# Optimization experiments

Hardware: AMD Instinct MI355X
Metric: run time of the kernel (lower is better)

The kernel has to match this reference:

```python
import jax, jax.numpy as jnp
import numpy as np

N_EMBD = 1024
N_HEAD = 16
LORA_R = 8
LORA_ALPHA = 16
SCALE = LORA_ALPHA / LORA_R


def lora_linear(x, W, b, A, Bm):
    # loralib: F.linear(x, W, b) + (x @ A.T @ B.T) * scaling
    return x @ W.T + b + ((x @ A.T) @ Bm.T) * SCALE


def setup_inputs() -> dict:
    key = jax.random.key(0)
    ks = jax.random.split(key, 9)
    B, T, C = 4, 2048, N_EMBD
    s_in = 1.0 / np.sqrt(C)
    x = jax.random.normal(ks[0], (B, T, C), dtype=jnp.float32)
    Wqkv = jax.random.normal(ks[1], (3 * C, C), dtype=jnp.float32) * s_in
    bqkv = jnp.zeros((3 * C,), dtype=jnp.float32)
    Aqkv = jax.random.normal(ks[2], (LORA_R, C), dtype=jnp.float32) * s_in
    Bqkv = jnp.zeros((3 * C, LORA_R), dtype=jnp.float32)  # loralib inits B to zero
    Wproj = jax.random.normal(ks[3], (C, C), dtype=jnp.float32) * s_in
    bproj = jnp.zeros((C,), dtype=jnp.float32)
    Aproj = jax.random.normal(ks[4], (LORA_R, C), dtype=jnp.float32) * s_in
    Bproj = jnp.zeros((C, LORA_R), dtype=jnp.float32)
    return {"x": x, "Wqkv": Wqkv, "bqkv": bqkv, "Aqkv": Aqkv, "Bqkv": Bqkv,
            "Wproj": Wproj, "bproj": bproj, "Aproj": Aproj, "Bproj": Bproj}


def reference(x, Wqkv, bqkv, Aqkv, Bqkv, Wproj, bproj, Aproj, Bproj):
    B, T, C = x.shape
    H, D = N_HEAD, C // N_HEAD
    qkv = lora_linear(x, Wqkv, bqkv, Aqkv, Bqkv)  # [B,T,3C]
    q, k, v = jnp.split(qkv, 3, axis=2)
    # [B,T,C] -> [B,H,T,D]
    q = q.reshape(B, T, H, D).transpose(0, 2, 1, 3)
    k = k.reshape(B, T, H, D).transpose(0, 2, 1, 3)
    v = v.reshape(B, T, H, D).transpose(0, 2, 1, 3)
    att = jnp.einsum("bhqd,bhkd->bhqk", q, k) * (1.0 / np.sqrt(D))
    causal = jnp.tril(jnp.ones((T, T), dtype=bool))
    att = jnp.where(causal[None, None], att, jnp.float32(-jnp.inf))
    att = jax.nn.softmax(att, axis=-1)
    out = jnp.einsum("bhqk,bhkd->bhqd", att, v)  # [B,H,T,D]
    out = out.transpose(0, 2, 1, 3).reshape(B, T, C)
    return lora_linear(out, Wproj, bproj, Aproj, Bproj)
```

## Files before the change

kernel.cpp:

```cpp
#include <hip/hip_runtime.h>
#include <hip/hip_bf16.h>

typedef __bf16 bf16_t;
typedef __bf16 bf16x8 __attribute__((ext_vector_type(8)));
typedef __bf16 bf16x4 __attribute__((ext_vector_type(4)));
typedef float  f32x4  __attribute__((ext_vector_type(4)));

#define MFMA_BF16 __builtin_amdgcn_mfma_f32_16x16x32_bf16
#define NEG_BIG  (-3.0e38f)

#if __has_builtin(__builtin_amdgcn_exp2f)
#define EXP2F(x) __builtin_amdgcn_exp2f(x)
#else
#define EXP2F(x) exp2f(x)
#endif

#define SBAR()       __builtin_amdgcn_s_barrier()
#define SCHED0()     __builtin_amdgcn_sched_barrier(0)
#define WAIT_LGKM0() asm volatile("s_waitcnt lgkmcnt(0)" ::: "memory")
#define WAIT_LGKM8() asm volatile("s_waitcnt lgkmcnt(8)" ::: "memory")
#define WAIT_VM0()   asm volatile("s_waitcnt vmcnt(0)" ::: "memory")
#define WAIT_VM4()   asm volatile("s_waitcnt vmcnt(4)" ::: "memory")
#define WAIT_VM6()   asm volatile("s_waitcnt vmcnt(6)" ::: "memory")

__device__ __forceinline__ void load16_lds(const bf16_t* g, bf16_t* l) {
    __builtin_amdgcn_global_load_lds(
        (const __attribute__((address_space(1))) void*)g,
        (__attribute__((address_space(3))) void*)l, 16, 0, 0);
}

__device__ inline bf16x8 ld8(const bf16_t* p) { return *(const bf16x8*)p; }
__device__ inline bf16x8 ld8(const float* p) {
    f32x4 a = *(const f32x4*)p;
    f32x4 b = *(const f32x4*)(p + 4);
    bf16x8 o;
    o[0] = (bf16_t)a[0]; o[1] = (bf16_t)a[1]; o[2] = (bf16_t)a[2]; o[3] = (bf16_t)a[3];
    o[4] = (bf16_t)b[0]; o[5] = (bf16_t)b[1]; o[6] = (bf16_t)b[2]; o[7] = (bf16_t)b[3];
    return o;
}

template <typename TX>
__device__ __forceinline__ void lora_xa_body(
    const TX* __restrict__ X, const float* __restrict__ A,
    float* __restrict__ out, int m, int lane)
{
    const TX* xp = X + (size_t)m * 1024;
    float acc[8];
#pragma unroll
    for (int r = 0; r < 8; r++) acc[r] = 0.f;

#pragma unroll 4
    for (int ci = 0; ci < 16; ci++) {
        int k = ci * 64 + lane;
        float xv = (float)xp[k];
#pragma unroll
        for (int r = 0; r < 8; r++) acc[r] += xv * A[r * 1024 + k];
    }
#pragma unroll
    for (int r = 0; r < 8; r++) {
        float v = acc[r];
        v += __shfl_xor(v, 1);  v += __shfl_xor(v, 2);  v += __shfl_xor(v, 4);
        v += __shfl_xor(v, 8);  v += __shfl_xor(v, 16); v += __shfl_xor(v, 32);
        if (lane == 0) out[m * 8 + r] = v;
    }
}

template <typename TX>
__global__ __launch_bounds__(256) void lora_xa_kernel(
    const TX* __restrict__ X, const float* __restrict__ A,
    float* __restrict__ out)
{
    const int lane = threadIdx.x & 63;
    const int w    = threadIdx.x >> 6;
    const int m    = blockIdx.x * 4 + w;
    lora_xa_body<TX>(X, A, out, m, lane);
}

__global__ __launch_bounds__(256) void prep_kernel(
    const float* __restrict__ x, const float* __restrict__ Wqkv,
    const float* __restrict__ Wproj,
    bf16_t* __restrict__ x16, bf16_t* __restrict__ Wqkv16,
    bf16_t* __restrict__ Wproj16,
    const float* __restrict__ Aqkv, float* __restrict__ xa1)
{
    const int bid = blockIdx.x;
    if (bid < 6144) {
        const float* in; bf16_t* out; size_t off;
        if (bid < 4096)      { in = x;     out = x16;     off = (size_t)bid * 2048; }
        else if (bid < 5632) { in = Wqkv;  out = Wqkv16;  off = (size_t)(bid - 4096) * 2048; }
        else                 { in = Wproj; out = Wproj16; off = (size_t)(bid - 5632) * 2048; }
        size_t i = off + (size_t)threadIdx.x * 8;
        *(bf16x8*)&out[i] = ld8(&in[i]);
    } else {
        const int lane = threadIdx.x & 63;
        const int w    = threadIdx.x >> 6;
        const int m    = (bid - 6144) * 4 + w;
        lora_xa_body<float>(x, Aqkv, xa1, m, lane);
    }
}

__device__ __forceinline__ void gemm_epilogue(
    f32x4 (&acc)[4][4], const float* bias, const float* xA, const float* LB,
    bf16_t* C0, bf16_t* C1, bf16_t* C2, float* Cf,
    int tile_m, int tile_n, int wm, int wn, int c, int g)
{
    const int seg    = tile_n >> 10;
    const int tn_loc = tile_n & 1023;
    bf16_t* Cout = (seg == 0) ? C0 : (seg == 1) ? C1 : C2;

    float biasf[4];
    float lbv[4][8];
#pragma unroll
    for (int j = 0; j < 4; j++) {
        int col = tile_n + wn + j * 16 + c;
        biasf[j] = bias[col];
        f32x4 lb0 = *(const f32x4*)&LB[(size_t)col * 8];
        f32x4 lb1 = *(const f32x4*)&LB[(size_t)col * 8 + 4];
#pragma unroll
        for (int r = 0; r < 4; r++) { lbv[j][r] = lb0[r]; lbv[j][r + 4] = lb1[r]; }
    }
#pragma unroll
    for (int i = 0; i < 4; i++) {
#pragma unroll
        for (int rg = 0; rg < 4; rg++) {
            int row = tile_m + wm + i * 16 + g * 4 + rg;
            f32x4 xa0 = *(const f32x4*)&xA[(size_t)row * 8];
            f32x4 xa1 = *(const f32x4*)&xA[(size_t)row * 8 + 4];
#pragma unroll
            for (int j = 0; j < 4; j++) {
                float lora = xa0[0] * lbv[j][0] + xa0[1] * lbv[j][1] +
                             xa0[2] * lbv[j][2] + xa0[3] * lbv[j][3] +
                             xa1[0] * lbv[j][4] + xa1[1] * lbv[j][5] +
                             xa1[2] * lbv[j][6] + xa1[3] * lbv[j][7];
                float v = acc[i][j][rg] + biasf[j] + 2.0f * lora;
                int lcol = tn_loc + wn + j * 16 + c;
                if (Cf) Cf[(size_t)row * 1024 + lcol] = v;
                else    Cout[(size_t)row * 1024 + lcol] = (bf16_t)v;
            }
        }
    }
}

template <typename TA, typename TW>
__global__ __launch_bounds__(256) void gemm_bias_lora(
    const TA* __restrict__ A, const TW* __restrict__ W,
    const float* __restrict__ bias, const float* __restrict__ xA,
    const float* __restrict__ LB,
    bf16_t* __restrict__ C0, bf16_t* __restrict__ C1, bf16_t* __restrict__ C2,
    float* __restrict__ Cf, int K)
{
    __shared__ __align__(16) bf16_t As[128 * 72];
    __shared__ __align__(16) bf16_t Bs[128 * 72];

    const int t    = threadIdx.x;
    const int lane = t & 63;
    const int w    = t >> 6;
    const int wm   = (w >> 1) * 64;
    const int wn   = (w & 1) * 64;
    const int c    = lane & 15;
    const int g    = lane >> 4;
    const int tile_m = blockIdx.y * 128;
    const int tile_n = blockIdx.x * 128;

    const int srow = t >> 3;
    const int scol = (t & 7) * 8;

    f32x4 acc[4][4];
#pragma unroll
    for (int i = 0; i < 4; i++)
#pragma unroll
        for (int j = 0; j < 4; j++) {
            f32x4 z = {0.f, 0.f, 0.f, 0.f};
            acc[i][j] = z;
        }

    for (int k0 = 0; k0 < K; k0 += 64) {
#pragma unroll
        for (int i = 0; i < 4; i++) {
            int r = srow + i * 32;
            *(bf16x8*)&As[r * 72 + scol] = ld8(&A[(size_t)(tile_m + r) * K + k0 + scol]);
            *(bf16x8*)&Bs[r * 72 + scol] = ld8(&W[(size_t)(tile_n + r) * K + k0 + scol]);
        }
        __syncthreads();

#pragma unroll
        for (int kk = 0; kk < 2; kk++) {
            bf16x8 af[4], bfr[4];
#pragma unroll
            for (int i = 0; i < 4; i++)
                af[i] = *(const bf16x8*)&As[(wm + i * 16 + c) * 72 + kk * 32 + g * 8];
#pragma unroll
            for (int j = 0; j < 4; j++)
                bfr[j] = *(const bf16x8*)&Bs[(wn + j * 16 + c) * 72 + kk * 32 + g * 8];
#pragma unroll
            for (int i = 0; i < 4; i++)
#pragma unroll
                for (int j = 0; j < 4; j++)
                    acc[i][j] = MFMA_BF16(af[i], bfr[j], acc[i][j], 0, 0, 0);
        }
        __syncthreads();
    }
    gemm_epilogue(acc, bias, xA, LB, C0, C1, C2, Cf, tile_m, tile_n, wm, wn, c, g);
}

#define AS_OFF(row, q) ((row) * 64 + (((q) ^ ((row) & 7)) * 8))

__global__ __launch_bounds__(256) void gemm_proj_fused(
    const bf16_t* __restrict__ A, const bf16_t* __restrict__ W,
    const float* __restrict__ bias, const float* __restrict__ Ap,
    const float* __restrict__ LB, float* __restrict__ Cf, int K)
{
    __shared__ __align__(16) bf16_t As[128 * 64];
    __shared__ __align__(16) bf16_t Bs[128 * 64];
    __shared__ __align__(16) bf16_t Ap16[8 * 1032];

    const int t    = threadIdx.x;
    const int lane = t & 63;
    const int w    = t >> 6;
    const int wm   = (w >> 1) * 64;
    const int wn   = (w & 1) * 64;
    const int c    = lane & 15;
    const int g    = lane >> 4;
    const int tile_m = blockIdx.y * 128;
    const int tile_n = blockIdx.x * 128;

    {
        int r = t >> 5;
        int k = (t & 31) * 32;
        const float* src = Ap + (size_t)r * 1024 + k;
        bf16_t* dst = &Ap16[r * 1032 + k];
#pragma unroll
        for (int e = 0; e < 32; e += 8)
            *(bf16x8*)&dst[e] = ld8(&src[e]);
    }

    const int trow = t >> 3;
    const int k8   = (t & 7) ^ (trow & 7);
    const bf16_t* Ab = A + (size_t)tile_m * K + k8 * 8;
    const bf16_t* Wb = W + (size_t)tile_n * K + k8 * 8;

    f32x4 acc[4][4];
#pragma unroll
    for (int i = 0; i < 4; i++)
#pragma unroll
        for (int j = 0; j < 4; j++) {
            f32x4 z = {0.f, 0.f, 0.f, 0.f};
            acc[i][j] = z;
        }
    f32x4 accx[2];
    {
        f32x4 z = {0.f, 0.f, 0.f, 0.f};
        accx[0] = z; accx[1] = z;
    }

    for (int k0 = 0; k0 < K; k0 += 64) {
#pragma unroll
        for (int i = 0; i < 4; i++) {
            int row = i * 32 + trow;
            load16_lds(&Ab[(size_t)row * K + k0], &As[(i * 256 + t) * 8]);
            load16_lds(&Wb[(size_t)row * K + k0], &Bs[(i * 256 + t) * 8]);
        }
        __syncthreads();

#pragma unroll
        for (int kk = 0; kk < 2; kk++) {
            bf16x8 af[4], bfr[4];
#pragma unroll
            for (int i = 0; i < 4; i++)
                af[i] = *(const bf16x8*)&As[AS_OFF(wm + i * 16 + c, kk * 4 + g)];
#pragma unroll
            for (int j = 0; j < 4; j++)
                bfr[j] = *(const bf16x8*)&Bs[AS_OFF(wn + j * 16 + c, kk * 4 + g)];
#pragma unroll
            for (int i = 0; i < 4; i++)
#pragma unroll
                for (int j = 0; j < 4; j++)
                    acc[i][j] = MFMA_BF16(af[i], bfr[j], acc[i][j], 0, 0, 0);
            bf16x8 apf = *(const bf16x8*)&Ap16[(c & 7) * 1032 + k0 + kk * 32 + g * 8];
#pragma unroll
            for (int fi = 0; fi < 2; fi++) {
                bf16x8 xf = *(const bf16x8*)&As[AS_OFF(w * 32 + fi * 16 + c, kk * 4 + g)];
                accx[fi] = MFMA_BF16(xf, apf, accx[fi], 0, 0, 0);
            }
        }
        __syncthreads();
    }

    float* xa2l = (float*)As;
    if (c < 8) {
#pragma unroll
        for (int fi = 0; fi < 2; fi++)
#pragma unroll
            for (int rg = 0; rg < 4; rg++)
                xa2l[(w * 32 + fi * 16 + g * 4 + rg) * 8 + c] = accx[fi][rg];
    }
    __syncthreads();

    float biasf[4];
    float lbv[4][8];
#pragma unroll
    for (int j = 0; j < 4; j++) {
        int col = tile_n + wn + j * 16 + c;
        biasf[j] = bias[col];
        f32x4 lb0 = *(const f32x4*)&LB[(size_t)col * 8];
        f32x4 lb1 = *(const f32x4*)&LB[(size_t)col * 8 + 4];
#pragma unroll
        for (int r = 0; r < 4; r++) { lbv[j][r] = lb0[r]; lbv[j][r + 4] = lb1[r]; }
    }
#pragma unroll
    for (int i = 0; i < 4; i++) {
#pragma unroll
        for (int rg = 0; rg < 4; rg++) {
            int rloc = wm + i * 16 + g * 4 + rg;
            int row  = tile_m + rloc;
            f32x4 xa0 = *(const f32x4*)&xa2l[rloc * 8];
            f32x4 xa1 = *(const f32x4*)&xa2l[rloc * 8 + 4];
#pragma unroll
            for (int j = 0; j < 4; j++) {
                float lora = xa0[0] * lbv[j][0] + xa0[1] * lbv[j][1] +
                             xa0[2] * lbv[j][2] + xa0[3] * lbv[j][3] +
                             xa1[0] * lbv[j][4] + xa1[1] * lbv[j][5] +
                             xa1[2] * lbv[j][6] + xa1[3] * lbv[j][7];
                float v = acc[i][j][rg] + biasf[j] + 2.0f * lora;
                Cf[(size_t)row * 1024 + tile_n + wn + j * 16 + c] = v;
            }
        }
    }
}

__global__ __launch_bounds__(512, 2) void gemm_256(
    const bf16_t* __restrict__ A, const bf16_t* __restrict__ W,
    const float* __restrict__ bias, const float* __restrict__ Aq,
    const float* __restrict__ LB,
    bf16_t* __restrict__ C0, bf16_t* __restrict__ C1, bf16_t* __restrict__ C2,
    float* __restrict__ Cf, int K, int ntn)
{
    __shared__ __align__(16) bf16_t As[4][8192];
    __shared__ __align__(16) bf16_t Bs[4][8192];
    __shared__ __align__(16) bf16_t Aq16[8 * 1032];

    const int t    = threadIdx.x;
    const int lane = t & 63;
    const int w    = t >> 6;
    const int c    = lane & 15;
    const int g    = lane >> 4;

    const int nwg = gridDim.x;
    const int cpx = nwg >> 3;
    const int bid = blockIdx.x;
    const int swz = (bid & 7) * cpx + (bid >> 3);
    const int tile_m = (swz / ntn) * 256;
    const int tile_n = (swz % ntn) * 256;

    const int wm  = (w >> 2) * 128;
    const int wn  = (w & 3) * 64;
    const int ha  = w >> 2;
    const int hb  = wn >> 7;
    const int wnl = wn & 127;

    {
        int r = t >> 6;
        int k = (t & 63) * 16;
        const float* src = Aq + (size_t)r * 1024 + k;
        bf16_t* dst = &Aq16[r * 1032 + k];
        *(bf16x8*)&dst[0] = ld8(&src[0]);
        *(bf16x8*)&dst[8] = ld8(&src[8]);
    }

    int aoffs[8][2], boffs[4][2];
#pragma unroll
    for (int il = 0; il < 8; il++) {
        int rl = il * 16 + c;
#pragma unroll
        for (int ks = 0; ks < 2; ks++)
            aoffs[il][ks] = rl * 64 + (((ks * 4 + g) ^ (rl & 7)) * 8);
    }
#pragma unroll
    for (int j2 = 0; j2 < 4; j2++) {
        int rl = wnl + j2 * 16 + c;
#pragma unroll
        for (int ks = 0; ks < 2; ks++)
            boffs[j2][ks] = rl * 64 + (((ks * 4 + g) ^ (rl & 7)) * 8);
    }

    const int xrow0 = (w & 3) * 32;
    int xoffs[2][2];
#pragma unroll
    for (int fi = 0; fi < 2; fi++) {
        int rl = xrow0 + fi * 16 + c;
#pragma unroll
        for (int ks = 0; ks < 2; ks++)
            xoffs[fi][ks] = rl * 64 + (((ks * 4 + g) ^ (rl & 7)) * 8);
    }

    const int trow = t >> 3;
    const int qq   = (t & 7) ^ (trow & 7);
    const bf16_t* aO = A + (size_t)(tile_m + trow) * K + qq * 8;
    const bf16_t* wO = W + (size_t)(tile_n + trow) * K + qq * 8;
    const size_t rK64 = (size_t)64 * K;

#define STAGE_A(T, h) do {                                                         \
    load16_lds(aO + (size_t)(h) * 128 * K + (size_t)(T) * 64,                      \
               &As[((T) & 1) * 2 + (h)][t * 8]);                                   \
    load16_lds(aO + (size_t)(h) * 128 * K + rK64 + (size_t)(T) * 64,               \
               &As[((T) & 1) * 2 + (h)][4096 + t * 8]); } while (0)
#define STAGE_B(T, h) do {                                                         \
    load16_lds(wO + (size_t)(h) * 128 * K + (size_t)(T) * 64,                      \
               &Bs[((T) & 1) * 2 + (h)][t * 8]);                                   \
    load16_lds(wO + (size_t)(h) * 128 * K + rK64 + (size_t)(T) * 64,               \
               &Bs[((T) & 1) * 2 + (h)][4096 + t * 8]); } while (0)

    f32x4 acc[8][4];
#pragma unroll
    for (int i = 0; i < 8; i++)
#pragma unroll
        for (int j2 = 0; j2 < 4; j2++) {
            f32x4 z = {0.f, 0.f, 0.f, 0.f};
            acc[i][j2] = z;
        }
    f32x4 accx[2];
    {
        f32x4 z = {0.f, 0.f, 0.f, 0.f};
        accx[0] = z; accx[1] = z;
    }

    const int NT = K >> 6;

    STAGE_B(0, 0); STAGE_B(0, 1); STAGE_A(0, 0); STAGE_A(0, 1);
    WAIT_VM4();
    STAGE_B(1, 0); STAGE_B(1, 1); STAGE_A(1, 0);
    WAIT_LGKM0();
    WAIT_VM6();
    SBAR();

    for (int j = 0; j < NT; j++) {
        const bf16_t* Ab = &As[(j & 1) * 2 + ha][0];
        const bf16_t* Bb = &Bs[(j & 1) * 2 + hb][0];
        bf16x8 bfr[4][2], af0[4], af1[4];
        bf16x8 xf0a, xf1a, xf0b, xf1b, apf0, apf1;

#pragma unroll
        for (int j2 = 0; j2 < 4; j2++) {
            bfr[j2][0] = *(const bf16x8*)&Bb[boffs[j2][0]];
            bfr[j2][1] = *(const bf16x8*)&Bb[boffs[j2][1]];
        }
#pragma unroll
        for (int i = 0; i < 4; i++) af0[i] = *(const bf16x8*)&Ab[aoffs[i][0]];
        if (j + 1 < NT) STAGE_A(j + 1, 1);
        WAIT_LGKM8();
        SBAR();
        WAIT_LGKM0();
        SCHED0();
        __builtin_amdgcn_s_setprio(1);
#pragma unroll
        for (int i = 0; i < 4; i++)
#pragma unroll
            for (int j2 = 0; j2 < 4; j2++)
                acc[i][j2] = MFMA_BF16(af0[i], bfr[j2][0], acc[i][j2], 0, 0, 0);
        __builtin_amdgcn_s_setprio(0);
        SBAR();

#pragma unroll
        for (int i = 0; i < 4; i++) af1[i] = *(const bf16x8*)&Ab[aoffs[i + 4][0]];
        xf0a = *(const bf16x8*)&Ab[xoffs[0][0]];
        xf1a = *(const bf16x8*)&Ab[xoffs[1][0]];
        apf0 = *(const bf16x8*)&Aq16[(c & 7) * 1032 + j * 64 + g * 8];
        if (j + 2 < NT) STAGE_B(j + 2, 0);
        SBAR();
        WAIT_LGKM0();
        SCHED0();
        __builtin_amdgcn_s_setprio(1);
#pragma unroll
        for (int i = 0; i < 4; i++)
#pragma unroll
            for (int j2 = 0; j2 < 4; j2++)
                acc[4 + i][j2] = MFMA_BF16(af1[i], bfr[j2][0], acc[4 + i][j2], 0, 0, 0);
        accx[0] = MFMA_BF16(xf0a, apf0, accx[0], 0, 0, 0);
        accx[1] = MFMA_BF16(xf1a, apf0, accx[1], 0, 0, 0);
        __builtin_amdgcn_s_setprio(0);
        SBAR();

#pragma unroll
        for (int i = 0; i < 4; i++) af0[i] = *(const bf16x8*)&Ab[aoffs[i][1]];
#pragma unroll
        for (int i = 0; i < 4; i++) af1[i] = *(const bf16x8*)&Ab[aoffs[i + 4][1]];
        xf0b = *(const bf16x8*)&Ab[xoffs[0][1]];
        xf1b = *(const bf16x8*)&Ab[xoffs[1][1]];
        apf1 = *(const bf16x8*)&Aq16[(c & 7) * 1032 + j * 64 + 32 + g * 8];
        if (j + 2 < NT) STAGE_B(j + 2, 1);
        SBAR();
        WAIT_LGKM0();
        SCHED0();
        __builtin_amdgcn_s_setprio(1);
#pragma unroll
        for (int i = 0; i < 4; i++)
#pragma unroll
            for (int j2 = 0; j2 < 4; j2++)
                acc[i][j2] = MFMA_BF16(af0[i], bfr[j2][1], acc[i][j2], 0, 0, 0);
        __builtin_amdgcn_s_setprio(0);
        SBAR();

        if (j + 2 < NT) STAGE_A(j + 2, 0);
        SBAR();
        __builtin_amdgcn_s_setprio(1);
#pragma unroll
        for (int i = 0; i < 4; i++)
#pragma unroll
            for (int j2 = 0; j2 < 4; j2++)
                acc[4 + i][j2] = MFMA_BF16(af1[i], bfr[j2][1], acc[4 + i][j2], 0, 0, 0);
        accx[0] = MFMA_BF16(xf0b, apf1, accx[0], 0, 0, 0);
        accx[1] = MFMA_BF16(xf1b, apf1, accx[1], 0, 0, 0);
        __builtin_amdgcn_s_setprio(0);
        if (j < NT - 2) WAIT_VM6(); else WAIT_VM0();
        SBAR();
    }
#undef STAGE_A
#undef STAGE_B

    float* xl = (float*)&As[0][0];
    if (c < 8) {
#pragma unroll
        for (int fi = 0; fi < 2; fi++)
#pragma unroll
            for (int rg = 0; rg < 4; rg++)
                xl[(ha * 128 + xrow0 + fi * 16 + g * 4 + rg) * 8 + c] = accx[fi][rg];
    }
    __syncthreads();

    const int seg    = tile_n >> 10;
    const int tn_loc = tile_n & 1023;
    bf16_t* Cout = (seg == 0) ? C0 : (seg == 1) ? C1 : C2;

    float biasf[4];
    float lbv[4][8];
#pragma unroll
    for (int j2 = 0; j2 < 4; j2++) {
        int col = tile_n + wn + j2 * 16 + c;
        biasf[j2] = bias[col];
        f32x4 lb0 = *(const f32x4*)&LB[(size_t)col * 8];
        f32x4 lb1 = *(const f32x4*)&LB[(size_t)col * 8 + 4];
#pragma unroll
        for (int r = 0; r < 4; r++) { lbv[j2][r] = lb0[r]; lbv[j2][r + 4] = lb1[r]; }
    }
#pragma unroll
    for (int i = 0; i < 8; i++) {
#pragma unroll
        for (int rg = 0; rg < 4; rg++) {
            int rloc = wm + i * 16 + g * 4 + rg;
            int row  = tile_m + rloc;
            f32x4 xa0 = *(const f32x4*)&xl[rloc * 8];
            f32x4 xa1 = *(const f32x4*)&xl[rloc * 8 + 4];
#pragma unroll
            for (int j2 = 0; j2 < 4; j2++) {
                float lora = xa0[0] * lbv[j2][0] + xa0[1] * lbv[j2][1] +
                             xa0[2] * lbv[j2][2] + xa0[3] * lbv[j2][3] +
                             xa1[0] * lbv[j2][4] + xa1[1] * lbv[j2][5] +
                             xa1[2] * lbv[j2][6] + xa1[3] * lbv[j2][7];
                float v = acc[i][j2][rg] + biasf[j2] + 2.0f * lora;
                int lcol = tn_loc + wn + j2 * 16 + c;
                if (Cf) Cf[(size_t)row * 1024 + lcol] = v;
                else    Cout[(size_t)row * 1024 + lcol] = (bf16_t)v;
            }
        }
    }
}

#define VT_IDX(d, kv) ((d) * 72 + ((d) >> 4) * 16 + (kv))
#define PS_IDX(q, kv) ((q) * 72 + ((q) >> 2) * 8 + (kv))
#define PW_REGION 1168

__global__ __launch_bounds__(256, 2) void attn_kernel(
    bf16_t* __restrict__ Q, const bf16_t* __restrict__ Kg,
    const bf16_t* __restrict__ Vg)
{
    __shared__ __align__(16) bf16_t Ks[64 * 72];
    __shared__ __align__(16) bf16_t Vt[64 * 72 + 64];
    __shared__ __align__(16) bf16_t Ps[8 * PW_REGION];

    const int t    = threadIdx.x;
    const int lane = t & 63;
    const int w    = t >> 6;
    const int c    = lane & 15;
    const int g    = lane >> 4;

    const int id = blockIdx.x;
    const int qb = 15 - (id >> 6);
    const int h  = id & 15;
    const int b  = (id >> 4) & 3;
    const int q0 = qb * 128;
    const size_t base = (size_t)b * 2048 * 1024;
    const int last = 2 * qb + 1;

    bf16x8 qfA[2], qfB[2];
    {
        const bf16_t* qpA = Q + base + (size_t)(q0 + w * 16 + c) * 1024 + h * 64;
        qfA[0] = *(const bf16x8*)&qpA[g * 8];
        qfA[1] = *(const bf16x8*)&qpA[32 + g * 8];
        const bf16_t* qpB = qpA + (size_t)64 * 1024;
        qfB[0] = *(const bf16x8*)&qpB[g * 8];
        qfB[1] = *(const bf16x8*)&qpB[32 + g * 8];
    }

    bf16x8 ones;
#pragma unroll
    for (int e = 0; e < 8; e++) ones[e] = (bf16_t)1.0f;

    f32x4 accA[4], accB[4];
#pragma unroll
    for (int jd = 0; jd < 4; jd++) {
        f32x4 z = {0.f, 0.f, 0.f, 0.f};
        accA[jd] = z; accB[jd] = z;
    }
    f32x4 lA = {0.f, 0.f, 0.f, 0.f};
    f32x4 lB = {0.f, 0.f, 0.f, 0.f};
    float mA = NEG_BIG, mB = NEG_BIG;

    const int sr = t >> 2;
    const int sc = (t & 3) * 16;
    const int vtbase = VT_IDX(sc, sr);

    bf16x8 kr0, kr1, vr0, vr1;
    {
        const bf16_t* kp = Kg + base + (size_t)sr * 1024 + h * 64 + sc;
        kr0 = *(const bf16x8*)&kp[0];
        kr1 = *(const bf16x8*)&kp[8];
        const bf16_t* vp = Vg + base + (size_t)sr * 1024 + h * 64 + sc;
        vr0 = *(const bf16x8*)&vp[0];
        vr1 = *(const bf16x8*)&vp[8];
    }

    bf16_t* PwA = &Ps[(w * 2 + 0) * PW_REGION];
    bf16_t* PwB = &Ps[(w * 2 + 1) * PW_REGION];
    const float SCL = 0.125f * 1.44269504088896f;

    for (int kt = 0; kt <= last; kt++) {
        if (kt > 0) __syncthreads();
        *(bf16x8*)&Ks[sr * 72 + sc]     = kr0;
        *(bf16x8*)&Ks[sr * 72 + sc + 8] = kr1;
#pragma unroll
        for (int e = 0; e < 8; e++) Vt[vtbase + e * 72]       = vr0[e];
#pragma unroll
        for (int e = 0; e < 8; e++) Vt[vtbase + (e + 8) * 72] = vr1[e];
        __syncthreads();

        if (kt < last) {
            const bf16_t* kp = Kg + base + (size_t)((kt + 1) * 64 + sr) * 1024 + h * 64 + sc;
            kr0 = *(const bf16x8*)&kp[0];
            kr1 = *(const bf16x8*)&kp[8];
            const bf16_t* vp = Vg + base + (size_t)((kt + 1) * 64 + sr) * 1024 + h * 64 + sc;
            vr0 = *(const bf16x8*)&vp[0];
            vr1 = *(const bf16x8*)&vp[8];
        }

        const bool doA = (kt <= 2 * qb);

        f32x4 sA[4], sB[4];
#pragma unroll
        for (int j = 0; j < 4; j++) {
            f32x4 z = {0.f, 0.f, 0.f, 0.f};
            sA[j] = z; sB[j] = z;
        }
#pragma unroll
        for (int kk = 0; kk < 2; kk++) {
            bf16x8 kf[4];
#pragma unroll
            for (int j = 0; j < 4; j++)
                kf[j] = *(const bf16x8*)&Ks[(j * 16 + c) * 72 + kk * 32 + g * 8];
            if (doA) {
#pragma unroll
                for (int j = 0; j < 4; j++)
                    sA[j] = MFMA_BF16(kf[j], qfA[kk], sA[j], 0, 0, 0);
            }
#pragma unroll
            for (int j = 0; j < 4; j++)
                sB[j] = MFMA_BF16(kf[j], qfB[kk], sB[j], 0, 0, 0);
        }

        if (doA) {
#pragma unroll
            for (int j = 0; j < 4; j++)
#pragma unroll
                for (int r = 0; r < 4; r++) sA[j][r] *= SCL;
            if (kt == 2 * qb) {
#pragma unroll
                for (int j = 0; j < 4; j++)
#pragma unroll
                    for (int r = 0; r < 4; r++)
                        if (j * 16 + g * 4 + r > w * 16 + c) sA[j][r] = NEG_BIG;
            }
            float mx;
            {
                float a0 = fmaxf(fmaxf(sA[0][0], sA[0][1]), fmaxf(sA[0][2], sA[0][3]));
                float a1 = fmaxf(fmaxf(sA[1][0], sA[1][1]), fmaxf(sA[1][2], sA[1][3]));
                float a2 = fmaxf(fmaxf(sA[2][0], sA[2][1]), fmaxf(sA[2][2], sA[2][3]));
                float a3 = fmaxf(fmaxf(sA[3][0], sA[3][1]), fmaxf(sA[3][2], sA[3][3]));
                mx = fmaxf(fmaxf(a0, a1), fmaxf(a2, a3));
                mx = fmaxf(mx, __shfl_xor(mx, 16));
                mx = fmaxf(mx, __shfl_xor(mx, 32));
            }
            if (!__all(mx <= mA + 8.0f)) {
                float mnew  = fmaxf(mA, mx);
                float alpha = EXP2F(mA - mnew);
                mA = mnew;
#pragma unroll
                for (int jd = 0; jd < 4; jd++)
#pragma unroll
                    for (int r = 0; r < 4; r++) accA[jd][r] *= alpha;
                lA[0] *= alpha;
            }
#pragma unroll
            for (int j = 0; j < 4; j++)
#pragma unroll
                for (int r = 0; r < 4; r++) sA[j][r] = EXP2F(sA[j][r] - mA);
#pragma unroll
            for (int j = 0; j < 4; j++) {
                bf16x4 pk;
#pragma unroll
                for (int r = 0; r < 4; r++) pk[r] = (bf16_t)sA[j][r];
                *(bf16x4*)&PwA[PS_IDX(c, j * 16 + g * 4)] = pk;
            }
        }

        {
#pragma unroll
            for (int j = 0; j < 4; j++)
#pragma unroll
                for (int r = 0; r < 4; r++) sB[j][r] *= SCL;
            if (kt == last) {
#pragma unroll
                for (int j = 0; j < 4; j++)
#pragma unroll
                    for (int r = 0; r < 4; r++)
                        if (j * 16 + g * 4 + r > w * 16 + c) sB[j][r] = NEG_BIG;
            }
            float mx;
            {
                float a0 = fmaxf(fmaxf(sB[0][0], sB[0][1]), fmaxf(sB[0][2], sB[0][3]));
                float a1 = fmaxf(fmaxf(sB[1][0], sB[1][1]), fmaxf(sB[1][2], sB[1][3]));
                float a2 = fmaxf(fmaxf(sB[2][0], sB[2][1]), fmaxf(sB[2][2], sB[2][3]));
                float a3 = fmaxf(fmaxf(sB[3][0], sB[3][1]), fmaxf(sB[3][2], sB[3][3]));
                mx = fmaxf(fmaxf(a0, a1), fmaxf(a2, a3));
                mx = fmaxf(mx, __shfl_xor(mx, 16));
                mx = fmaxf(mx, __shfl_xor(mx, 32));
            }
            if (!__all(mx <= mB + 8.0f)) {
                float mnew  = fmaxf(mB, mx);
                float alpha = EXP2F(mB - mnew);
                mB = mnew;
#pragma unroll
                for (int jd = 0; jd < 4; jd++)
#pragma unroll
                    for (int r = 0; r < 4; r++) accB[jd][r] *= alpha;
                lB[0] *= alpha;
            }
#pragma unroll
            for (int j = 0; j < 4; j++)
#pragma unroll
                for (int r = 0; r < 4; r++) sB[j][r] = EXP2F(sB[j][r] - mB);
#pragma unroll
            for (int j = 0; j < 4; j++) {
                bf16x4 pk;
#pragma unroll
                for (int r = 0; r < 4; r++) pk[r] = (bf16_t)sB[j][r];
                *(bf16x4*)&PwB[PS_IDX(c, j * 16 + g * 4)] = pk;
            }
        }

#pragma unroll
        for (int kkv = 0; kkv < 2; kkv++) {
            bf16x8 vf[4];
#pragma unroll
            for (int jd = 0; jd < 4; jd++)
                vf[jd] = *(const bf16x8*)&Vt[VT_IDX(jd * 16 + c, kkv * 32 + g * 8)];
            if (doA) {
                bf16x8 pfA = *(const bf16x8*)&PwA[PS_IDX(c, kkv * 32 + g * 8)];
#pragma unroll
                for (int jd = 0; jd < 4; jd++)
                    accA[jd] = MFMA_BF16(vf[jd], pfA, accA[jd], 0, 0, 0);
                lA = MFMA_BF16(ones, pfA, lA, 0, 0, 0);
            }
            bf16x8 pfB = *(const bf16x8*)&PwB[PS_IDX(c, kkv * 32 + g * 8)];
#pragma unroll
            for (int jd = 0; jd < 4; jd++)
                accB[jd] = MFMA_BF16(vf[jd], pfB, accB[jd], 0, 0, 0);
            lB = MFMA_BF16(ones, pfB, lB, 0, 0, 0);
        }
    }

    {
        float rl = 1.0f / lA[0];
        bf16_t* op = Q + base + (size_t)(q0 + w * 16 + c) * 1024 + h * 64;
#pragma unroll
        for (int jd = 0; jd < 4; jd++) {
            bf16x4 o4;
#pragma unroll
            for (int r = 0; r < 4; r++) o4[r] = (bf16_t)(accA[jd][r] * rl);
            *(bf16x4*)&op[jd * 16 + g * 4] = o4;
        }
    }
    {
        float rl = 1.0f / lB[0];
        bf16_t* op = Q + base + (size_t)(q0 + 64 + w * 16 + c) * 1024 + h * 64;
#pragma unroll
        for (int jd = 0; jd < 4; jd++) {
            bf16x4 o4;
#pragma unroll
            for (int r = 0; r < 4; r++) o4[r] = (bf16_t)(accB[jd][r] * rl);
            *(bf16x4*)&op[jd * 16 + g * 4] = o4;
        }
    }
}

extern "C" void kernel_launch(void* const* d_in, const int* in_sizes, int n_in,
                              void* d_out, int out_size, void* d_ws, size_t ws_size,
                              hipStream_t stream) {
    const float* x     = (const float*)d_in[0];
    const float* Wqkv  = (const float*)d_in[1];
    const float* bqkv  = (const float*)d_in[2];
    const float* Aqkv  = (const float*)d_in[3];
    const float* Bqkv  = (const float*)d_in[4];
    const float* Wproj = (const float*)d_in[5];
    const float* bproj = (const float*)d_in[6];
    const float* Aproj = (const float*)d_in[7];
    const float* Bproj = (const float*)d_in[8];
    float* out = (float*)d_out;

    char* ws = (char*)d_ws;
    const bool big = ws_size >= (size_t)(72.5 * 1024 * 1024) + 65536;

    if (big) {
        float*  xa1    = (float*)ws;
        bf16_t* x16    = (bf16_t*)(ws + 524288);
        bf16_t* Wqkv16 = x16 + (size_t)8192 * 1024;
        bf16_t* Wproj16= Wqkv16 + (size_t)3072 * 1024;
        bf16_t* Qfull  = Wproj16 + (size_t)1024 * 1024;
        bf16_t* Kfull  = Qfull + (size_t)8192 * 1024;
        bf16_t* Vfull  = Kfull + (size_t)8192 * 1024;

        prep_kernel<<<6144, 256, 0, stream>>>(
            x, Wqkv, Wproj, x16, Wqkv16, Wproj16, Aqkv, xa1);

        gemm_256<<<384, 512, 0, stream>>>(
            x16, Wqkv16, bqkv, Aqkv, Bqkv, Qfull, Kfull, Vfull, nullptr, 1024, 12);

        attn_kernel<<<1024, 256, 0, stream>>>(Qfull, Kfull, Vfull);

        gemm_proj_fused<<<dim3(8, 64), 256, 0, stream>>>(
            Qfull, Wproj16, bproj, Aproj, Bproj, out, 1024);
    } else {
        float*  xa1   = (float*)ws;
        float*  xa2   = (float*)(ws + 262144);
        bf16_t* Qfull = (bf16_t*)(ws + 524288);
        bf16_t* Kfull = Qfull + (size_t)8192 * 1024;
        bf16_t* Vfull = Kfull + (size_t)8192 * 1024;

        lora_xa_kernel<float><<<2048, 256, 0, stream>>>(x, Aqkv, xa1);
        gemm_bias_lora<float, float><<<dim3(24, 64), 256, 0, stream>>>(
            x, Wqkv, bqkv, xa1, Bqkv, Qfull, Kfull, Vfull, nullptr, 1024);
        attn_kernel<<<1024, 256, 0, stream>>>(Qfull, Kfull, Vfull);
        lora_xa_kernel<bf16_t><<<2048, 256, 0, stream>>>(Qfull, Aproj, xa2);
        gemm_bias_lora<bf16_t, float><<<dim3(8, 64), 256, 0, stream>>>(
            Qfull, Wproj, bproj, xa2, Bproj,
            nullptr, nullptr, nullptr, out, 1024);
    }
}
```

Before: 289.1 us.

## Widen attention KV tile from 64 to 128 keys per iteration

The attention kernel now processes 128 keys per loop iteration instead of 64. This halves the number of barrier-synchronised iterations and the staging round-trips through LDS. It drops the per-iteration doA branch, so the A-half query rows compute on every tile and masking handles the diagonal. The cost is more LDS (bigger K, V-transposed and P buffers), higher register pressure from 8 score fragments per half, and some wasted MFMA work on the last tile for the A rows.

```diff
diff --git a/kernel.cpp b/kernel.cpp
--- a/kernel.cpp
+++ b/kernel.cpp
@@ -565,16 +565,16 @@
     }
 }
 
-#define VT_IDX(d, kv) ((d) * 72 + ((d) >> 4) * 16 + (kv))
-#define PS_IDX(q, kv) ((q) * 72 + ((q) >> 2) * 8 + (kv))
-#define PW_REGION 1168
+#define VT_IDX(d, kv) ((d) * 136 + ((d) >> 4) * 16 + (kv))
+#define PS_IDX(q, kv) ((q) * 136 + ((q) >> 2) * 8 + (kv))
+#define PW_REGION 2208
 
 __global__ __launch_bounds__(256, 2) void attn_kernel(
     bf16_t* __restrict__ Q, const bf16_t* __restrict__ Kg,
     const bf16_t* __restrict__ Vg)
 {
-    __shared__ __align__(16) bf16_t Ks[64 * 72];
-    __shared__ __align__(16) bf16_t Vt[64 * 72 + 64];
+    __shared__ __align__(16) bf16_t Ks[128 * 72];
+    __shared__ __align__(16) bf16_t Vt[64 * 136 + 64];
     __shared__ __align__(16) bf16_t Ps[8 * PW_REGION];
 
     const int t    = threadIdx.x;
@@ -589,7 +589,6 @@
     const int b  = (id >> 4) & 3;
     const int q0 = qb * 128;
     const size_t base = (size_t)b * 2048 * 1024;
-    const int last = 2 * qb + 1;
 
     bf16x8 qfA[2], qfB[2];
     {
@@ -615,89 +614,88 @@
     f32x4 lB = {0.f, 0.f, 0.f, 0.f};
     float mA = NEG_BIG, mB = NEG_BIG;
 
-    const int sr = t >> 2;
-    const int sc = (t & 3) * 16;
-    const int vtbase = VT_IDX(sc, sr);
-
-    bf16x8 kr0, kr1, vr0, vr1;
+    const int sr  = t >> 1;
+    const int sc2 = (t & 1) * 32;
+
+    bf16x8 kr[4], vr[4];
     {
-        const bf16_t* kp = Kg + base + (size_t)sr * 1024 + h * 64 + sc;
-        kr0 = *(const bf16x8*)&kp[0];
-        kr1 = *(const bf16x8*)&kp[8];
-        const bf16_t* vp = Vg + base + (size_t)sr * 1024 + h * 64 + sc;
-        vr0 = *(const bf16x8*)&vp[0];
-        vr1 = *(const bf16x8*)&vp[8];
+        const bf16_t* kp = Kg + base + (size_t)sr * 1024 + h * 64 + sc2;
+        const bf16_t* vp = Vg + base + (size_t)sr * 1024 + h * 64 + sc2;
+#pragma unroll
+        for (int e = 0; e < 4; e++) {
+            kr[e] = *(const bf16x8*)&kp[e * 8];
+            vr[e] = *(const bf16x8*)&vp[e * 8];
+        }
     }
 
     bf16_t* PwA = &Ps[(w * 2 + 0) * PW_REGION];
     bf16_t* PwB = &Ps[(w * 2 + 1) * PW_REGION];
     const float SCL = 0.125f * 1.44269504088896f;
 
-    for (int kt = 0; kt <= last; kt++) {
+    for (int kt = 0; kt <= qb; kt++) {
         if (kt > 0) __syncthreads();
-        *(bf16x8*)&Ks[sr * 72 + sc]     = kr0;
-        *(bf16x8*)&Ks[sr * 72 + sc + 8] = kr1;
-#pragma unroll
-        for (int e = 0; e < 8; e++) Vt[vtbase + e * 72]       = vr0[e];
-#pragma unroll
-        for (int e = 0; e < 8; e++) Vt[vtbase + (e + 8) * 72] = vr1[e];
+#pragma unroll
+        for (int e = 0; e < 4; e++)
+            *(bf16x8*)&Ks[sr * 72 + sc2 + e * 8] = kr[e];
+#pragma unroll
+        for (int ee = 0; ee < 4; ee++)
+#pragma unroll
+            for (int e2 = 0; e2 < 8; e2++) {
+                int d = sc2 + ee * 8 + e2;
+                Vt[VT_IDX(d, sr)] = vr[ee][e2];
+            }
         __syncthreads();
 
-        if (kt < last) {
-            const bf16_t* kp = Kg + base + (size_t)((kt + 1) * 64 + sr) * 1024 + h * 64 + sc;
-            kr0 = *(const bf16x8*)&kp[0];
-            kr1 = *(const bf16x8*)&kp[8];
-            const bf16_t* vp = Vg + base + (size_t)((kt + 1) * 64 + sr) * 1024 + h * 64 + sc;
-            vr0 = *(const bf16x8*)&vp[0];
-            vr1 = *(const bf16x8*)&vp[8];
-        }
-
-        const bool doA = (kt <= 2 * qb);
-
-        f32x4 sA[4], sB[4];
-#pragma unroll
-        for (int j = 0; j < 4; j++) {
+        if (kt < qb) {
+            const bf16_t* kp = Kg + base + (size_t)((kt + 1) * 128 + sr) * 1024 + h * 64 + sc2;
+            const bf16_t* vp = Vg + base + (size_t)((kt + 1) * 128 + sr) * 1024 + h * 64 + sc2;
+#pragma unroll
+            for (int e = 0; e < 4; e++) {
+                kr[e] = *(const bf16x8*)&kp[e * 8];
+                vr[e] = *(const bf16x8*)&vp[e * 8];
+            }
+        }
+
+        f32x4 sA[8], sB[8];
+#pragma unroll
+        for (int j = 0; j < 8; j++) {
             f32x4 z = {0.f, 0.f, 0.f, 0.f};
             sA[j] = z; sB[j] = z;
         }
 #pragma unroll
         for (int kk = 0; kk < 2; kk++) {
-            bf16x8 kf[4];
-#pragma unroll
-            for (int j = 0; j < 4; j++)
-                kf[j] = *(const bf16x8*)&Ks[(j * 16 + c) * 72 + kk * 32 + g * 8];
-            if (doA) {
-#pragma unroll
-                for (int j = 0; j < 4; j++)
-                    sA[j] = MFMA_BF16(kf[j], qfA[kk], sA[j], 0, 0, 0);
-            }
-#pragma unroll
-            for (int j = 0; j < 4; j++)
-                sB[j] = MFMA_BF16(kf[j], qfB[kk], sB[j], 0, 0, 0);
-        }
-
-        if (doA) {
-#pragma unroll
-            for (int j = 0; j < 4; j++)
-#pragma unroll
-                for (int r = 0; r < 4; r++) sA[j][r] *= SCL;
-            if (kt == 2 * qb) {
-#pragma unroll
-                for (int j = 0; j < 4; j++)
-#pragma unroll
-                    for (int r = 0; r < 4; r++)
-                        if (j * 16 + g * 4 + r > w * 16 + c) sA[j][r] = NEG_BIG;
-            }
-            float mx;
-            {
-                float a0 = fmaxf(fmaxf(sA[0][0], sA[0][1]), fmaxf(sA[0][2], sA[0][3]));
-                float a1 = fmaxf(fmaxf(sA[1][0], sA[1][1]), fmaxf(sA[1][2], sA[1][3]));
-                float a2 = fmaxf(fmaxf(sA[2][0], sA[2][1]), fmaxf(sA[2][2], sA[2][3]));
-                float a3 = fmaxf(fmaxf(sA[3][0], sA[3][1]), fmaxf(sA[3][2], sA[3][3]));
-                mx = fmaxf(fmaxf(a0, a1), fmaxf(a2, a3));
-                mx = fmaxf(mx, __shfl_xor(mx, 16));
-                mx = fmaxf(mx, __shfl_xor(mx, 32));
-            }
+#pragma unroll
+            for (int j = 0; j < 8; j++) {
+                bf16x8 kf = *(const bf16x8*)&Ks[(j * 16 + c) * 72 + kk * 32 + g * 8];
+                sA[j] = MFMA_BF16(kf, qfA[kk], sA[j], 0, 0, 0);
+                sB[j] = MFMA_BF16(kf, qfB[kk], sB[j], 0, 0, 0);
+            }
+        }
+
+#pragma unroll
+        for (int j = 0; j < 8; j++)
+#pragma unroll
+            for (int r = 0; r < 4; r++) { sA[j][r] *= SCL; sB[j][r] *= SCL; }
+
+        if (kt == qb) {
+#pragma unroll
+            for (int j = 0; j < 8; j++)
+#pragma unroll
+                for (int r = 0; r < 4; r++) {
+                    int kvl = j * 16 + g * 4 + r;
+                    if (kvl > w * 16 + c)      sA[j][r] = NEG_BIG;
+                    if (kvl > 64 + w * 16 + c) sB[j][r] = NEG_BIG;
+                }
+        }
+
+        {
+            float mx = sA[0][0];
+#pragma unroll
+            for (int j = 0; j < 8; j++)
+#pragma unroll
+                for (int r = 0; r < 4; r++) mx = fmaxf(mx, sA[j][r]);
+            mx = fmaxf(mx, __shfl_xor(mx, 16));
+            mx = fmaxf(mx, __shfl_xor(mx, 32));
             if (!__all(mx <= mA + 8.0f)) {
                 float mnew  = fmaxf(mA, mx);
                 float alpha = EXP2F(mA - mnew);
@@ -709,11 +707,11 @@
                 lA[0] *= alpha;
             }
 #pragma unroll
-            for (int j = 0; j < 4; j++)
+            for (int j = 0; j < 8; j++)
 #pragma unroll
                 for (int r = 0; r < 4; r++) sA[j][r] = EXP2F(sA[j][r] - mA);
 #pragma unroll
-            for (int j = 0; j < 4; j++) {
+            for (int j = 0; j < 8; j++) {
                 bf16x4 pk;
 #pragma unroll
                 for (int r = 0; r < 4; r++) pk[r] = (bf16_t)sA[j][r];
@@ -722,27 +720,13 @@
         }
 
         {
-#pragma unroll
-            for (int j = 0; j < 4; j++)
-#pragma unroll
-                for (int r = 0; r < 4; r++) sB[j][r] *= SCL;
-            if (kt == last) {
-#pragma unroll
-                for (int j = 0; j < 4; j++)
-#pragma unroll
-                    for (int r = 0; r < 4; r++)
-                        if (j * 16 + g * 4 + r > w * 16 + c) sB[j][r] = NEG_BIG;
-            }
-            float mx;
-            {
-                float a0 = fmaxf(fmaxf(sB[0][0], sB[0][1]), fmaxf(sB[0][2], sB[0][3]));
-                float a1 = fmaxf(fmaxf(sB[1][0], sB[1][1]), fmaxf(sB[1][2], sB[1][3]));
-                float a2 = fmaxf(fmaxf(sB[2][0], sB[2][1]), fmaxf(sB[2][2], sB[2][3]));
-                float a3 = fmaxf(fmaxf(sB[3][0], sB[3][1]), fmaxf(sB[3][2], sB[3][3]));
-                mx = fmaxf(fmaxf(a0, a1), fmaxf(a2, a3));
-                mx = fmaxf(mx, __shfl_xor(mx, 16));
-                mx = fmaxf(mx, __shfl_xor(mx, 32));
-            }
+            float mx = sB[0][0];
+#pragma unroll
+            for (int j = 0; j < 8; j++)
+#pragma unroll
+                for (int r = 0; r < 4; r++) mx = fmaxf(mx, sB[j][r]);
+            mx = fmaxf(mx, __shfl_xor(mx, 16));
+            mx = fmaxf(mx, __shfl_xor(mx, 32));
             if (!__all(mx <= mB + 8.0f)) {
                 float mnew  = fmaxf(mB, mx);
                 float alpha = EXP2F(mB - mnew);
@@ -754,11 +738,11 @@
                 lB[0] *= alpha;
             }
 #pragma unroll
-            for (int j = 0; j < 4; j++)
+            for (int j = 0; j < 8; j++)
 #pragma unroll
                 for (int r = 0; r < 4; r++) sB[j][r] = EXP2F(sB[j][r] - mB);
 #pragma unroll
-            for (int j = 0; j < 4; j++) {
+            for (int j = 0; j < 8; j++) {
                 bf16x4 pk;
 #pragma unroll
                 for (int r = 0; r < 4; r++) pk[r] = (bf16_t)sB[j][r];
@@ -767,22 +751,16 @@
         }
 
 #pragma unroll
-        for (int kkv = 0; kkv < 2; kkv++) {
-            bf16x8 vf[4];
-#pragma unroll
-            for (int jd = 0; jd < 4; jd++)
-                vf[jd] = *(const bf16x8*)&Vt[VT_IDX(jd * 16 + c, kkv * 32 + g * 8)];
-            if (doA) {
-                bf16x8 pfA = *(const bf16x8*)&PwA[PS_IDX(c, kkv * 32 + g * 8)];
-#pragma unroll
-                for (int jd = 0; jd < 4; jd++)
-                    accA[jd] = MFMA_BF16(vf[jd], pfA, accA[jd], 0, 0, 0);
-                lA = MFMA_BF16(ones, pfA, lA, 0, 0, 0);
-            }
+        for (int kkv = 0; kkv < 4; kkv++) {
+            bf16x8 pfA = *(const bf16x8*)&PwA[PS_IDX(c, kkv * 32 + g * 8)];
             bf16x8 pfB = *(const bf16x8*)&PwB[PS_IDX(c, kkv * 32 + g * 8)];
 #pragma unroll
-            for (int jd = 0; jd < 4; jd++)
-                accB[jd] = MFMA_BF16(vf[jd], pfB, accB[jd], 0, 0, 0);
+            for (int jd = 0; jd < 4; jd++) {
+                bf16x8 vf = *(const bf16x8*)&Vt[VT_IDX(jd * 16 + c, kkv * 32 + g * 8)];
+                accA[jd] = MFMA_BF16(vf, pfA, accA[jd], 0, 0, 0);
+                accB[jd] = MFMA_BF16(vf, pfB, accB[jd], 0, 0, 0);
+            }
+            lA = MFMA_BF16(ones, pfA, lA, 0, 0, 0);
             lB = MFMA_BF16(ones, pfB, lB, 0, 0, 0);
         }
     }
```

Result: no change. 285.8 us (-1.2%).
